# Kernel optimization log

Measured on AMD Instinct MI355X. Metric: run time of the kernel, lower is better.

The kernel has to match this reference:

```python
import jax, jax.numpy as jnp
import numpy as np

NUM_EMBEDDINGS = 1024
EMBEDDING_DIM = 64
COMMITMENT_COST = 0.25
N_TOKENS = 131072  # e.g. batch 128 of 32x32 latent grids, flattened


def setup_inputs() -> dict:
    key = jax.random.key(0)
    k1, k2 = jax.random.split(key)
    z_e = jax.random.normal(k1, (N_TOKENS, EMBEDDING_DIM), dtype=jnp.float32)
    # torch init: uniform_(-1/K, 1/K)
    lim = 1.0 / NUM_EMBEDDINGS
    embeddings = jax.random.uniform(
        k2, (NUM_EMBEDDINGS, EMBEDDING_DIM), dtype=jnp.float32,
        minval=-lim, maxval=lim)
    return {"z_e": z_e, "embeddings": embeddings}


def reference(z_e, embeddings):
    # Squared L2 distances via the expanded form: ||z||^2 - 2 z.E^T + ||e||^2.
    # Same math as sum((z[:,None,:]-E[None,:,:])**2, -1) without the (N,K,D)
    # intermediate; only additive constants per-row, so argmin is identical.
    z_sq = jnp.sum(z_e * z_e, axis=1, keepdims=True)           # [N,1]
    e_sq = jnp.sum(embeddings * embeddings, axis=1)            # [K]
    distances = z_sq - 2.0 * (z_e @ embeddings.T) + e_sq[None, :]  # [N,K]
    encoding_indices = jnp.argmin(distances, axis=1)           # [N] int
    z_q = embeddings[encoding_indices]                         # [N,D]

    sg = jax.lax.stop_gradient
    codebook_loss = jnp.mean((sg(z_q) - z_e) ** 2)
    commit_loss = jnp.mean((z_q - sg(z_e)) ** 2)
    vq_loss = codebook_loss + COMMITMENT_COST * commit_loss

    # Straight-through estimator
    z_q_st = z_e + sg(z_q - z_e)
    return z_q_st, vq_loss, encoding_indices
```

## Files before the change

kernel.cpp:

```cpp
#include <hip/hip_runtime.h>

#define NTOK   131072
#define KCODES 1024
#define DIM    64
#define BM     128
#define BN     128
#define NCT    (KCODES / BN)
#define SLOT_CAP 16384

#define LOSS_OFF (NTOK * DIM)
#define IDX_OFF  (LOSS_OFF + 1)

#define EPS_U 3e-5f

typedef __attribute__((ext_vector_type(8))) short bf16x8;
typedef __attribute__((ext_vector_type(4))) float f32x4;
typedef __attribute__((ext_vector_type(4))) unsigned short ush4;

#if defined(__has_builtin)
#if __has_builtin(__builtin_amdgcn_global_load_lds)
#define HAVE_GLD 1
#endif
#endif

#ifdef HAVE_GLD
typedef const __attribute__((address_space(1))) unsigned int* gas_u32p;
typedef __attribute__((address_space(3))) unsigned int* las_u32p;
#define GLD16(ldst, gsrc) \
    __builtin_amdgcn_global_load_lds((gas_u32p)(gsrc), (las_u32p)(ldst), 16, 0, 0)
#endif

__device__ inline unsigned short bf16rtn(float x) {
    unsigned u = __float_as_uint(x);
    return (unsigned short)((u + 0x7fffu + ((u >> 16) & 1u)) >> 16);
}

__device__ inline unsigned long long packdi(float d, int idx) {
    unsigned b = __float_as_uint(d);
    b ^= (b & 0x80000000u) ? 0xFFFFFFFFu : 0x80000000u;
    return ((unsigned long long)b << 32) | (unsigned)idx;
}

__global__ __launch_bounds__(256) void prep_kernel(const float* __restrict__ E,
                                                   unsigned short* __restrict__ Bswz,
                                                   float* __restrict__ esqh,
                                                   float* __restrict__ esq,
                                                   int* __restrict__ cnt) {
    const int t = threadIdx.x, b = blockIdx.x;
    if (b == 0 && t == 0) cnt[0] = 0;
    int id = b * 256 + t;
    int c = id >> 6, k = id & 63;
    float x = E[id];
    unsigned short h = bf16rtn(x);
    float hf = __uint_as_float(((unsigned)h) << 16);
    unsigned short lo = bf16rtn(x - hf);
    int rx = (c & 7) << 4;
    int qh = (k >> 3) << 4;
    int ob = (k & 7) << 1;
    Bswz[(c * 256 + (qh ^ rx) + ob) >> 1]           = h;
    Bswz[(c * 256 + ((128 + qh) ^ rx) + ob) >> 1]   = lo;
    if (b < 4) {
        int cc = b * 256 + t;
        const float4* row = (const float4*)(E + cc * DIM);
        float s = 0.f;
        #pragma unroll
        for (int i = 0; i < DIM / 4; ++i) {
            float4 v = row[i];
            s += v.x * v.x + v.y * v.y + v.z * v.z + v.w * v.w;
        }
        esq[cc] = s;
        esqh[cc] = 0.5f * s;
    }
}

__global__ __launch_bounds__(512, 4) void mfma_argmin_kernel(
    const float* __restrict__ z, const float* __restrict__ E,
    const unsigned short* __restrict__ Bswz, const float* __restrict__ esqh_g,
    float* __restrict__ idx_out, float* __restrict__ out0,
    float* __restrict__ partials, int* __restrict__ cnt, int* __restrict__ wl,
    unsigned long long* __restrict__ bitmap) {
    __shared__ __align__(16) char lds[65536];
    __shared__ __align__(16) char aux[4096];
    float* esqh_s  = (float*)aux;
    float* cb_best = (float*)aux;
    float* cb_sec  = (float*)(aux + 1024);
    int*   cb_idx  = (int*)(aux + 2048);
    int*   fbi     = (int*)(aux + 3072);
    float* wred    = (float*)(aux + 3584);

    const int t = threadIdx.x;
    const int l = t & 63;
    const int w = t >> 6;
    const int rg = w >> 1;
    const int cg = w & 1;
    const int lan15 = l & 15;
    const int kp16 = (l >> 4) * 16;
    const int xr = (lan15 & 7) << 4;
    const int row0 = blockIdx.x * BM;
    const char* gb = (const char*)Bswz;

#ifdef HAVE_GLD
    #pragma unroll
    for (int p = 0; p < 4; ++p)
        GLD16(lds + 32768 + p * 8192 + t * 16, gb + p * 8192 + t * 16);
#else
    uint4 pv0[4];
    #pragma unroll
    for (int p = 0; p < 4; ++p)
        pv0[p] = *(const uint4*)(gb + p * 8192 + t * 16);
#endif

    esqh_s[t]       = esqh_g[t];
    esqh_s[512 + t] = esqh_g[512 + t];

    {
        const float4* zg = (const float4*)(z + (size_t)row0 * DIM);
        float4 av[4];
        #pragma unroll
        for (int p = 0; p < 4; ++p) av[p] = zg[p * 512 + t];
        #pragma unroll
        for (int p = 0; p < 4; ++p) {
            int li = p * 512 + t;
            int r = li >> 4, q = li & 15;
            float xs[4] = {av[p].x, av[p].y, av[p].z, av[p].w};
            ush4 hv, lv;
            #pragma unroll
            for (int j = 0; j < 4; ++j) {
                unsigned short h = bf16rtn(xs[j]);
                float hf = __uint_as_float(((unsigned)h) << 16);
                hv[j] = h;
                lv[j] = bf16rtn(xs[j] - hf);
            }
            int rxw = (r & 7) << 4;
            int o = ((q * 8) ^ rxw);
            *(ush4*)(lds + r * 128 + o)         = hv;
            *(ush4*)(lds + 16384 + r * 128 + o) = lv;
        }
    }
#ifndef HAVE_GLD
    #pragma unroll
    for (int p = 0; p < 4; ++p)
        *(uint4*)(lds + 32768 + p * 8192 + t * 16) = pv0[p];
#endif
    __syncthreads();

    const int ko0 = kp16 ^ xr;
    const int ko1 = (64 + kp16) ^ xr;
    const int arow = (rg * 32 + lan15) * 128;

    bf16x8 ah00 = *(const bf16x8*)(lds + arow + ko0);
    bf16x8 ah01 = *(const bf16x8*)(lds + arow + ko1);
    bf16x8 ah10 = *(const bf16x8*)(lds + arow + 2048 + ko0);
    bf16x8 ah11 = *(const bf16x8*)(lds + arow + 2048 + ko1);
    bf16x8 al00 = *(const bf16x8*)(lds + 16384 + arow + ko0);
    bf16x8 al01 = *(const bf16x8*)(lds + 16384 + arow + ko1);
    bf16x8 al10 = *(const bf16x8*)(lds + 16384 + arow + 2048 + ko0);
    bf16x8 al11 = *(const bf16x8*)(lds + 16384 + arow + 2048 + ko1);
    __syncthreads();

    float best[8], second[8];
    int   bidx[8];
    #pragma unroll
    for (int s = 0; s < 8; ++s) { best[s] = 3.4e38f; second[s] = 3.4e38f; bidx[s] = 0; }

    const int brow = (cg * 64 + lan15) * 256;

    for (int ct = 0; ct < NCT; ++ct) {
        char* cur = lds + ((ct & 1) ^ 1) * 32768;
        if (ct < NCT - 1) {
            char* nbuf = lds + (ct & 1) * 32768;
            const char* g = gb + (size_t)(ct + 1) * 32768;
#ifdef HAVE_GLD
            #pragma unroll
            for (int p = 0; p < 4; ++p)
                GLD16(nbuf + p * 8192 + t * 16, g + p * 8192 + t * 16);
#else
            #pragma unroll
            for (int p = 0; p < 4; ++p)
                *(uint4*)(nbuf + p * 8192 + t * 16) =
                    *(const uint4*)(g + p * 8192 + t * 16);
#endif
        }

        f32x4 acc[2][4];
        #pragma unroll
        for (int fr = 0; fr < 2; ++fr)
            #pragma unroll
            for (int fc = 0; fc < 4; ++fc)
                acc[fr][fc] = (f32x4){0.f, 0.f, 0.f, 0.f};

        #pragma unroll
        for (int fc = 0; fc < 4; ++fc) {
            const char* bp = cur + brow + fc * 4096;
            bf16x8 b0 = *(const bf16x8*)(bp + ko0);
            bf16x8 b1 = *(const bf16x8*)(bp + ko1);
            acc[0][fc] = __builtin_amdgcn_mfma_f32_16x16x32_bf16(ah00, b0, acc[0][fc], 0, 0, 0);
            acc[1][fc] = __builtin_amdgcn_mfma_f32_16x16x32_bf16(ah10, b0, acc[1][fc], 0, 0, 0);
            acc[0][fc] = __builtin_amdgcn_mfma_f32_16x16x32_bf16(ah01, b1, acc[0][fc], 0, 0, 0);
            acc[1][fc] = __builtin_amdgcn_mfma_f32_16x16x32_bf16(ah11, b1, acc[1][fc], 0, 0, 0);
            acc[0][fc] = __builtin_amdgcn_mfma_f32_16x16x32_bf16(al00, b0, acc[0][fc], 0, 0, 0);
            acc[1][fc] = __builtin_amdgcn_mfma_f32_16x16x32_bf16(al10, b0, acc[1][fc], 0, 0, 0);
            acc[0][fc] = __builtin_amdgcn_mfma_f32_16x16x32_bf16(al01, b1, acc[0][fc], 0, 0, 0);
            acc[1][fc] = __builtin_amdgcn_mfma_f32_16x16x32_bf16(al11, b1, acc[1][fc], 0, 0, 0);
            {
                bf16x8 b2 = *(const bf16x8*)(bp + 128 + ko0);
                acc[0][fc] = __builtin_amdgcn_mfma_f32_16x16x32_bf16(ah00, b2, acc[0][fc], 0, 0, 0);
                acc[1][fc] = __builtin_amdgcn_mfma_f32_16x16x32_bf16(ah10, b2, acc[1][fc], 0, 0, 0);
            }
            {
                bf16x8 b3 = *(const bf16x8*)(bp + 128 + ko1);
                acc[0][fc] = __builtin_amdgcn_mfma_f32_16x16x32_bf16(ah01, b3, acc[0][fc], 0, 0, 0);
                acc[1][fc] = __builtin_amdgcn_mfma_f32_16x16x32_bf16(ah11, b3, acc[1][fc], 0, 0, 0);
            }
        }

        #pragma unroll
        for (int fc = 0; fc < 4; ++fc) {
            int col = ct * BN + cg * 64 + fc * 16 + lan15;
            float eh = esqh_s[col];
            #pragma unroll
            for (int fr = 0; fr < 2; ++fr) {
                #pragma unroll
                for (int r = 0; r < 4; ++r) {
                    float u = eh - acc[fr][fc][r];
                    int s = fr * 4 + r;
                    second[s] = fminf(second[s], fmaxf(u, best[s]));
                    bidx[s] = (u < best[s]) ? col : bidx[s];
                    best[s] = fminf(u, best[s]);
                }
            }
        }
        __syncthreads();
    }

    #pragma unroll
    for (int s = 0; s < 8; ++s) {
        float b = best[s], sc = second[s];
        int bi = bidx[s];
        #pragma unroll
        for (int off = 1; off <= 8; off <<= 1) {
            float ob = __shfl_xor(b, off);
            float os = __shfl_xor(sc, off);
            int   oi = __shfl_xor(bi, off);
            float mx = fmaxf(b, ob);
            sc = fminf(fminf(sc, os), mx);
            if (ob < b) { b = ob; bi = oi; }
            else if (ob == b) bi = min(bi, oi);
        }
        best[s] = b; second[s] = sc; bidx[s] = bi;
    }
    if (lan15 == 0) {
        #pragma unroll
        for (int s = 0; s < 8; ++s) {
            int row = rg * 32 + (s >> 2) * 16 + (l >> 4) * 4 + (s & 3);
            cb_best[cg * BM + row] = best[s];
            cb_sec [cg * BM + row] = second[s];
            cb_idx [cg * BM + row] = bidx[s];
        }
    }
    __syncthreads();
    if (t < BM) {
        float b0 = cb_best[t], b1 = cb_best[BM + t];
        float s0 = cb_sec[t],  s1 = cb_sec[BM + t];
        int   i0 = cb_idx[t],  i1 = cb_idx[BM + t];
        float b; int bi;
        if (b1 < b0 || (b1 == b0 && i1 < i0)) { b = b1; bi = i1; }
        else                                  { b = b0; bi = i0; }
        float sec = fminf(fminf(s0, s1), fmaxf(b0, b1));
        int gid = row0 + t;
        idx_out[gid] = (float)bi;
        bool flg = (sec - b <= EPS_U);
        fbi[t] = bi | (flg ? 0x80000000 : 0);
        unsigned long long mask = __ballot(flg);
        if (l == 0) bitmap[blockIdx.x * 2 + w] = mask;
        int nf = __popcll(mask);
        int base = 0;
        if (l == 0 && nf) base = atomicAdd(cnt, nf);
        base = __shfl(base, 0);
        if (flg) {
            int pos = __popcll(mask & ((1ull << l) - 1ull));
            int slot = base + pos;
            if (slot < SLOT_CAP) wl[slot] = gid;
        }
    }
    __syncthreads();

    {
        const int tk = t >> 2, qd = t & 3;
        int pk = fbi[tk];
        int bi = pk & 0x3FF;
        bool fl = pk < 0;
        const float4* zr = (const float4*)z + (size_t)(row0 + tk) * 16 + qd * 4;
        const float4* er = (const float4*)E + (size_t)bi * 16 + qd * 4;
        float4* orow = (float4*)out0 + (size_t)(row0 + tk) * 16 + qd * 4;
        float ls = 0.f;
        #pragma unroll
        for (int j = 0; j < 4; ++j) {
            float4 zv = zr[j], ev = er[j];
            float dx = ev.x - zv.x, dy = ev.y - zv.y;
            float dz = ev.z - zv.z, dw = ev.w - zv.w;
            float4 o = {zv.x + dx, zv.y + dy, zv.z + dz, zv.w + dw};
            orow[j] = o;
            ls += dx * dx + dy * dy + dz * dz + dw * dw;
        }
        if (fl) ls = 0.f;
        #pragma unroll
        for (int off = 1; off <= 32; off <<= 1) ls += __shfl_xor(ls, off);
        if (l == 0) wred[w] = ls;
    }
    __syncthreads();
    if (t == 0) {
        float s = 0.f;
        #pragma unroll
        for (int i = 0; i < 8; ++i) s += wred[i];
        partials[blockIdx.x] = s;
    }
}

__global__ __launch_bounds__(256) void fallback_kernel(
    const float* __restrict__ z, const float* __restrict__ E,
    const float* __restrict__ esq_g, unsigned long long* __restrict__ cand,
    const int* __restrict__ wl, const int* __restrict__ cnt_p) {
    __shared__ __align__(16) float es[DIM][128];
    __shared__ __align__(16) float zl[16][72];
    __shared__ float zqs[16];

    const int t = threadIdx.x;
    const int tg = t >> 4;
    const int cs = t & 15;
    const int cnt = min(*cnt_p, SLOT_CAP);
    const int nwork = ((cnt + 15) >> 4) << 2;

    for (int cb = blockIdx.x; cb < nwork; cb += 2048) {
        const int chunk = cb >> 2, qtr = cb & 3;
        const int base = chunk * 16;
        const int nval = min(16, cnt - base);
        const int tok = wl[base + (tg < nval ? tg : 0)];
        {
            float4 v = ((const float4*)z)[(size_t)tok * 16 + cs];
            *(float4*)&zl[tg][cs * 4] = v;
        }
        __syncthreads();
        if (t < 16) {
            float s = 0.f;
            for (int k = 0; k < DIM; ++k) { float v = zl[t][k]; s += v * v; }
            zqs[t] = s;
        }
        __syncthreads();
        const float zq = zqs[tg];

        float best = 3.4e38f;
        int bi = 0;
        for (int ti = 0; ti < 2; ++ti) {
            const int tile = qtr * 2 + ti;
            const float4* eg = (const float4*)(E + (size_t)tile * 128 * DIM);
            #pragma unroll
            for (int p = 0; p < 8; ++p) {
                int li = p * 256 + t;
                int c = li & 127, k4 = li >> 7;
                float4 v = eg[c * 16 + k4];
                es[k4 * 4 + 0][c] = v.x;
                es[k4 * 4 + 1][c] = v.y;
                es[k4 * 4 + 2][c] = v.z;
                es[k4 * 4 + 3][c] = v.w;
            }
            __syncthreads();

            float acc[8];
            #pragma unroll
            for (int n = 0; n < 8; ++n) acc[n] = 0.f;
            #pragma unroll 8
            for (int k = 0; k < DIM; ++k) {
                float a = zl[tg][k];
                float4 b0 = *(const float4*)&es[k][cs * 8 + 0];
                float4 b1 = *(const float4*)&es[k][cs * 8 + 4];
                float b[8] = {b0.x, b0.y, b0.z, b0.w, b1.x, b1.y, b1.z, b1.w};
                #pragma unroll
                for (int n = 0; n < 8; ++n) acc[n] += a * b[n];
            }
            #pragma unroll
            for (int n = 0; n < 8; ++n) {
                int c = tile * 128 + cs * 8 + n;
                float d = (zq - 2.0f * acc[n]) + esq_g[c];
                if (d < best) { best = d; bi = c; }
            }
            __syncthreads();
        }
        #pragma unroll
        for (int off = 1; off <= 8; off <<= 1) {
            float ob = __shfl_xor(best, off);
            int   oi = __shfl_xor(bi, off);
            if (ob < best || (ob == best && oi < bi)) { best = ob; bi = oi; }
        }
        if (cs == 0 && tg < nval)
            cand[(size_t)(base + tg) * 4 + qtr] = packdi(best, bi);
        __syncthreads();
    }
}

__global__ __launch_bounds__(256) void repair_kernel(
    const float* __restrict__ z, const float* __restrict__ E,
    float* __restrict__ idx_out, float* __restrict__ out0,
    float* __restrict__ contrib, const unsigned long long* __restrict__ cand,
    const int* __restrict__ wl, const int* __restrict__ cnt_p) {
    const int t = threadIdx.x;
    const int tg = t >> 4;
    const int cs = t & 15;
    const int cnt = min(*cnt_p, SLOT_CAP);

    for (int s0 = blockIdx.x * 16; s0 < cnt; s0 += 512 * 16) {
        int s = s0 + tg;
        if (s < cnt) {
            int tok = wl[s];
            unsigned long long m = cand[(size_t)s * 4 + 0];
            m = min(m, cand[(size_t)s * 4 + 1]);
            m = min(m, cand[(size_t)s * 4 + 2]);
            m = min(m, cand[(size_t)s * 4 + 3]);
            int bi = (int)(unsigned)(m & 0xFFFFFFFFull);
            float4 zv = ((const float4*)z)[(size_t)tok * 16 + cs];
            float4 ev = ((const float4*)E)[(size_t)bi * 16 + cs];
            float dx = ev.x - zv.x, dy = ev.y - zv.y;
            float dz = ev.z - zv.z, dw = ev.w - zv.w;
            float4 o = {zv.x + dx, zv.y + dy, zv.z + dz, zv.w + dw};
            ((float4*)out0)[(size_t)tok * 16 + cs] = o;
            float c4 = dx * dx + dy * dy + dz * dz + dw * dw;
            #pragma unroll
            for (int off = 1; off <= 8; off <<= 1) c4 += __shfl_xor(c4, off);
            if (cs == 0) {
                idx_out[tok] = (float)bi;
                contrib[tok] = c4;
            }
        }
    }
}

__global__ __launch_bounds__(256) void loss_kernel(
    const float* __restrict__ partials, const unsigned long long* __restrict__ bitmap,
    const float* __restrict__ contrib, float* __restrict__ loss_out) {
    __shared__ float red[256];
    const int t = threadIdx.x;
    float p = 0.f;
    #pragma unroll
    for (int i = 0; i < 4; ++i) p += partials[t * 4 + i];
    for (int wi = t * 8; wi < t * 8 + 8; ++wi) {
        unsigned long long m = bitmap[wi];
        while (m) {
            int b = __builtin_ctzll(m);
            p += contrib[wi * 64 + b];
            m &= m - 1;
        }
    }
    red[t] = p;
    __syncthreads();
    for (int s = 128; s >= 1; s >>= 1) {
        if (t < s) red[t] += red[t + s];
        __syncthreads();
    }
    if (t == 0) {
        float m = red[0] / (float)(NTOK * DIM);
        loss_out[0] = m + 0.25f * m;
    }
}

extern "C" void kernel_launch(void* const* d_in, const int* in_sizes, int n_in,
                              void* d_out, int out_size, void* d_ws, size_t ws_size,
                              hipStream_t stream) {
    const float* z = (const float*)d_in[0];
    const float* E = (const float*)d_in[1];
    float* out = (float*)d_out;

    char* wsb = (char*)d_ws;
    float*              esq      = (float*)(wsb);
    float*              esqh     = (float*)(wsb + 4096);
    float*              partials = (float*)(wsb + 8192);
    int*                cnt      = (int*)(wsb + 16384);
    int*                wl       = (int*)(wsb + 20480);
    unsigned long long* bitmap   = (unsigned long long*)(wsb + 86016);
    unsigned short*     Bswz     = (unsigned short*)(wsb + 102400);
    float*              contrib  = (float*)(wsb + 364544);
    unsigned long long* cand     = (unsigned long long*)(wsb + 888832);

    prep_kernel<<<256, 256, 0, stream>>>(E, Bswz, esqh, esq, cnt);
    mfma_argmin_kernel<<<NTOK / BM, 512, 0, stream>>>(z, E, Bswz, esqh,
                                                      out + IDX_OFF, out,
                                                      partials, cnt, wl, bitmap);
    fallback_kernel<<<2048, 256, 0, stream>>>(z, E, esq, cand, wl, cnt);
    repair_kernel<<<512, 256, 0, stream>>>(z, E, out + IDX_OFF, out, contrib,
                                           cand, wl, cnt);
    loss_kernel<<<1, 256, 0, stream>>>(partials, bitmap, contrib, out + LOSS_OFF);
}
```

Before: 120.0 us.

## Use triple-buffered 64-code tiles with prefetch depth two and manual waitcnt barriers

Halves the codebook tile width to 64 codes and rotates three LDS buffers so global-to-LDS loads run two tiles ahead. The full __syncthreads is replaced by a selective s_waitcnt vmcnt plus s_barrier, and the loop is fully unrolled. The second-best update now uses a single med3 instruction. The intent is to hide load latency better and cut LDS use from 64KB to 48KB so more blocks fit per CU. In exchange there are twice as many barriers and less MFMA work per barrier.

```diff
diff --git a/kernel.cpp b/kernel.cpp
--- a/kernel.cpp
+++ b/kernel.cpp
@@ -4,7 +4,7 @@
 #define KCODES 1024
 #define DIM    64
 #define BM     128
-#define BN     128
+#define BN     64
 #define NCT    (KCODES / BN)
 #define SLOT_CAP 16384
 
@@ -21,6 +21,12 @@
 #if __has_builtin(__builtin_amdgcn_global_load_lds)
 #define HAVE_GLD 1
 #endif
+#if __has_builtin(__builtin_amdgcn_fmed3f)
+#define MED3(a,b,c) __builtin_amdgcn_fmed3f((a),(b),(c))
+#endif
+#endif
+#ifndef MED3
+#define MED3(a,b,c) fminf((a), fmaxf((b),(c)))
 #endif
 
 #ifdef HAVE_GLD
@@ -79,7 +85,7 @@
     float* __restrict__ idx_out, float* __restrict__ out0,
     float* __restrict__ partials, int* __restrict__ cnt, int* __restrict__ wl,
     unsigned long long* __restrict__ bitmap) {
-    __shared__ __align__(16) char lds[65536];
+    __shared__ __align__(16) char lds[49152];
     __shared__ __align__(16) char aux[4096];
     float* esqh_s  = (float*)aux;
     float* cb_best = (float*)aux;
@@ -99,17 +105,6 @@
     const int row0 = blockIdx.x * BM;
     const char* gb = (const char*)Bswz;
 
-#ifdef HAVE_GLD
-    #pragma unroll
-    for (int p = 0; p < 4; ++p)
-        GLD16(lds + 32768 + p * 8192 + t * 16, gb + p * 8192 + t * 16);
-#else
-    uint4 pv0[4];
-    #pragma unroll
-    for (int p = 0; p < 4; ++p)
-        pv0[p] = *(const uint4*)(gb + p * 8192 + t * 16);
-#endif
-
     esqh_s[t]       = esqh_g[t];
     esqh_s[512 + t] = esqh_g[512 + t];
 
@@ -137,11 +132,6 @@
             *(ush4*)(lds + 16384 + r * 128 + o) = lv;
         }
     }
-#ifndef HAVE_GLD
-    #pragma unroll
-    for (int p = 0; p < 4; ++p)
-        *(uint4*)(lds + 32768 + p * 8192 + t * 16) = pv0[p];
-#endif
     __syncthreads();
 
     const int ko0 = kp16 ^ xr;
@@ -158,39 +148,57 @@
     bf16x8 al11 = *(const bf16x8*)(lds + 16384 + arow + 2048 + ko1);
     __syncthreads();
 
+#ifdef HAVE_GLD
+    GLD16(lds + t * 16,         gb + t * 16);
+    GLD16(lds + 8192 + t * 16,  gb + 8192 + t * 16);
+    GLD16(lds + 16384 + t * 16, gb + 16384 + t * 16);
+    GLD16(lds + 24576 + t * 16, gb + 24576 + t * 16);
+    asm volatile("s_waitcnt vmcnt(2)" ::: "memory");
+    __builtin_amdgcn_sched_barrier(0);
+    __builtin_amdgcn_s_barrier();
+    __builtin_amdgcn_sched_barrier(0);
+#else
+    #pragma unroll
+    for (int p = 0; p < 4; ++p)
+        *(uint4*)(lds + p * 8192 + t * 16) = *(const uint4*)(gb + p * 8192 + t * 16);
+    __syncthreads();
+#endif
+
     float best[8], second[8];
     int   bidx[8];
     #pragma unroll
     for (int s = 0; s < 8; ++s) { best[s] = 3.4e38f; second[s] = 3.4e38f; bidx[s] = 0; }
 
-    const int brow = (cg * 64 + lan15) * 256;
-
+    const int brow = (cg * 32 + lan15) * 256;
+
+    #pragma unroll
     for (int ct = 0; ct < NCT; ++ct) {
-        char* cur = lds + ((ct & 1) ^ 1) * 32768;
-        if (ct < NCT - 1) {
-            char* nbuf = lds + (ct & 1) * 32768;
-            const char* g = gb + (size_t)(ct + 1) * 32768;
+        const char* cur = lds + (ct % 3) * 16384;
 #ifdef HAVE_GLD
-            #pragma unroll
-            for (int p = 0; p < 4; ++p)
-                GLD16(nbuf + p * 8192 + t * 16, g + p * 8192 + t * 16);
+        if (ct < NCT - 2) {
+            char* nbuf = lds + ((ct + 2) % 3) * 16384;
+            const char* g = gb + (size_t)(ct + 2) * 16384;
+            GLD16(nbuf + t * 16,        g + t * 16);
+            GLD16(nbuf + 8192 + t * 16, g + 8192 + t * 16);
+        }
 #else
-            #pragma unroll
-            for (int p = 0; p < 4; ++p)
-                *(uint4*)(nbuf + p * 8192 + t * 16) =
-                    *(const uint4*)(g + p * 8192 + t * 16);
-#endif
-        }
-
-        f32x4 acc[2][4];
+        uint4 pva, pvb;
+        if (ct < NCT - 2) {
+            const char* g = gb + (size_t)(ct + 2) * 16384;
+            pva = *(const uint4*)(g + t * 16);
+            pvb = *(const uint4*)(g + 8192 + t * 16);
+        }
+#endif
+
+        f32x4 acc[2][2];
         #pragma unroll
         for (int fr = 0; fr < 2; ++fr)
             #pragma unroll
-            for (int fc = 0; fc < 4; ++fc)
+            for (int fc = 0; fc < 2; ++fc)
                 acc[fr][fc] = (f32x4){0.f, 0.f, 0.f, 0.f};
 
         #pragma unroll
-        for (int fc = 0; fc < 4; ++fc) {
+        for (int fc = 0; fc < 2; ++fc) {
             const char* bp = cur + brow + fc * 4096;
             bf16x8 b0 = *(const bf16x8*)(bp + ko0);
             bf16x8 b1 = *(const bf16x8*)(bp + ko1);
@@ -215,8 +223,8 @@
         }
 
         #pragma unroll
-        for (int fc = 0; fc < 4; ++fc) {
-            int col = ct * BN + cg * 64 + fc * 16 + lan15;
+        for (int fc = 0; fc < 2; ++fc) {
+            int col = ct * BN + cg * 32 + fc * 16 + lan15;
             float eh = esqh_s[col];
             #pragma unroll
             for (int fr = 0; fr < 2; ++fr) {
@@ -224,13 +232,33 @@
                 for (int r = 0; r < 4; ++r) {
                     float u = eh - acc[fr][fc][r];
                     int s = fr * 4 + r;
-                    second[s] = fminf(second[s], fmaxf(u, best[s]));
+                    second[s] = MED3(second[s], u, best[s]);
                     bidx[s] = (u < best[s]) ? col : bidx[s];
                     best[s] = fminf(u, best[s]);
                 }
             }
         }
+
+#ifdef HAVE_GLD
+        if (ct < NCT - 2) {
+            asm volatile("s_waitcnt vmcnt(2) lgkmcnt(0)" ::: "memory");
+        } else if (ct == NCT - 2) {
+            asm volatile("s_waitcnt vmcnt(0) lgkmcnt(0)" ::: "memory");
+        } else {
+            asm volatile("s_waitcnt lgkmcnt(0)" ::: "memory");
+        }
+        __builtin_amdgcn_sched_barrier(0);
+        __builtin_amdgcn_s_barrier();
+        __builtin_amdgcn_sched_barrier(0);
+#else
         __syncthreads();
+        if (ct < NCT - 2) {
+            char* nbuf = lds + ((ct + 2) % 3) * 16384;
+            *(uint4*)(nbuf + t * 16)        = pva;
+            *(uint4*)(nbuf + 8192 + t * 16) = pvb;
+        }
+        __syncthreads();
+#endif
     }
 
     #pragma unroll
```

Measured after the change: 389.5 us. 3.25x slower.
